# Optimization experiments

Measured on AMD Instinct MI355X. Metric: run time of the kernel, lower is better.

The kernel has to match this reference:

```python
import jax, jax.numpy as jnp
import numpy as np
from jax import lax

EPS = 1e-5

def conv2d(x, w, b, pad):
    y = lax.conv_general_dilated(x, w, (1, 1), [(pad, pad), (pad, pad)],
                                 dimension_numbers=('NCHW', 'OIHW', 'NCHW'))
    return y + b[None, :, None, None]

def batchnorm(x, gamma, beta):
    # training-mode BN (nn.Module default): biased batch stats over N,H,W
    m = x.mean((0, 2, 3), keepdims=True)
    v = x.var((0, 2, 3), keepdims=True)
    return (x - m) * lax.rsqrt(v + EPS) * gamma[None, :, None, None] + beta[None, :, None, None]

def mish(x):
    return x * jnp.tanh(jax.nn.softplus(x))

def haar_dwt2(y):
    # pywt.dwt2(..., 'haar', mode='zero') for even H,W: 2x2 block transform.
    # cA='aa', cH='da' (detail along rows axis), cV='ad', cD='dd'; scale 1/2.
    a = y[..., 0::2, 0::2]
    b = y[..., 0::2, 1::2]
    c = y[..., 1::2, 0::2]
    d = y[..., 1::2, 1::2]
    cA = (a + b + c + d) * 0.5
    cH = (a + b - c - d) * 0.5
    cV = (a - b + c - d) * 0.5
    cD = (a - b - c + d) * 0.5
    return cA, cH, cV, cD

def setup_inputs() -> dict:
    key = jax.random.key(0)
    ks = jax.random.split(key, 8)
    C = 64
    x = jax.random.normal(ks[0], (8, C, 256, 256), dtype=jnp.float32)
    def kaiming(k, shape):
        fan_in = int(np.prod(shape[1:]))
        return jax.random.normal(k, shape, dtype=jnp.float32) / np.sqrt(fan_in)
    return {
        'x': x,
        'w1': kaiming(ks[1], (2 * C, C, 3, 3)), 'b1': jnp.zeros((2 * C,), jnp.float32),
        'g1': jnp.ones((2 * C,), jnp.float32), 'be1': jnp.zeros((2 * C,), jnp.float32),
        'w2': kaiming(ks[2], (C, 2 * C, 3, 3)), 'b2': jnp.zeros((C,), jnp.float32),
        'g2': jnp.ones((C,), jnp.float32), 'be2': jnp.zeros((C,), jnp.float32),
        'wh': kaiming(ks[3], (C, 3 * C, 1, 1)), 'bh': jnp.zeros((C,), jnp.float32),
        'gh': jnp.ones((C,), jnp.float32), 'beh': jnp.zeros((C,), jnp.float32),
    }

def reference(x, w1, b1, g1, be1, w2, b2, g2, be2, wh, bh, gh, beh):
    residual = x
    h = mish(batchnorm(conv2d(x, w1, b1, 1), g1, be1))
    h = mish(batchnorm(conv2d(h, w2, b2, 1), g2, be2))
    y = h + residual
    # original SS_Block detaches before the DWT
    y = lax.stop_gradient(y)
    cA, cH, cV, cD = haar_dwt2(y)
    x_low = cA
    x_high = jnp.concatenate([cH, cV, cD], axis=1)  # [B, 3C, H/2, W/2]
    x_high = mish(batchnorm(conv2d(x_high, wh, bh, 0), gh, beh))
    return (x_low, x_high)
```

## Files before the change

kernel.cpp:

```cpp
#include <hip/hip_runtime.h>
#include <hip/hip_bf16.h>

#define DEV static __device__ __forceinline__

typedef short v8s __attribute__((ext_vector_type(8)));
typedef float v4f __attribute__((ext_vector_type(4)));
typedef unsigned short v4u __attribute__((ext_vector_type(4)));

constexpr int N_ = 8;
constexpr float EPS_ = 1e-5f;
constexpr float INV_CNT = 1.f / 524288.f;
constexpr int CHB = 12800;

constexpr int PB1 = 0;
constexpr int PB2 = 262144;
constexpr int PBH = 327680;


__device__ __align__(16) unsigned short g_wT1[9*128*64];
__device__ __align__(16) unsigned short g_wT2[9*64*128];
__device__ __align__(16) unsigned short g_whT[64*192];
__device__ __align__(16) float g_stats[512];
__device__ __align__(16) float g_part[458752];
__device__ __align__(16) unsigned short g_zero[64];

DEV float bfbits2f(unsigned short u) { return __uint_as_float(((unsigned)u) << 16); }
DEV unsigned short f2bfbits(float f) {
    __hip_bfloat16 h = __float2bfloat16(f);
    unsigned short b;
    __builtin_memcpy(&b, &h, 2);
    return b;
}

DEV float mishf(float v) {
    float t = __expf(fminf(v, 30.f));
    float num = fmaf(t, t, 2.f * t);
    return v * num * __builtin_amdgcn_rcpf(num + 2.f);
}

DEV void gll16(const unsigned short* g, unsigned short* l) {
    __builtin_amdgcn_global_load_lds(
        (const __attribute__((address_space(1))) unsigned int*)g,
        (__attribute__((address_space(3))) unsigned int*)l,
        16, 0, 0);
}

__global__ __launch_bounds__(256) void prep(const float* __restrict__ w1,
                                            const float* __restrict__ w2,
                                            const float* __restrict__ wh)
{
    int idx = blockIdx.x * 256 + threadIdx.x;
    if (idx < 512) g_stats[idx] = 0.f;
    if (idx < 64) g_zero[idx] = 0;
    if (idx < 12288) g_whT[idx] = f2bfbits(wh[idx]);
    if (idx < 73728) {
        int tap = idx / 8192, rem = idx & 8191;
        {   int oc = rem >> 6, ic = rem & 63;
            g_wT1[idx] = f2bfbits(w1[(oc * 64 + ic) * 9 + tap]); }
        {   int oc = rem >> 7, ic = rem & 127;
            g_wT2[idx] = f2bfbits(w2[(oc * 128 + ic) * 9 + tap]); }
    }
}

__global__ __launch_bounds__(256) void transpose_x(const float* __restrict__ x,
                                                   unsigned short* __restrict__ xh)
{
    __shared__ float t[64][65];
    const int tid = threadIdx.x;
    const int bid = blockIdx.x;
    const int n = bid >> 10, pb = bid & 1023;
    const size_t pix0 = (size_t)pb * 64;
    const float* xb = x + ((size_t)n << 22) + pix0;
#pragma unroll
    for (int cb = 0; cb < 4; ++cb) {
        int c = (tid >> 4) + cb * 16;
        int p = (tid & 15) * 4;
        float4 v = *(const float4*)(xb + ((size_t)c << 16) + p);
        t[c][p] = v.x; t[c][p+1] = v.y; t[c][p+2] = v.z; t[c][p+3] = v.w;
    }
    __syncthreads();
    unsigned short* ob = xh + (((size_t)n << 16) + pix0) * 64;
#pragma unroll
    for (int pb2 = 0; pb2 < 2; ++pb2) {
        int p = (tid >> 3) + pb2 * 32;
        int c0 = (tid & 7) * 8;
        v8s r;
#pragma unroll
        for (int i = 0; i < 8; ++i) r[i] = (short)f2bfbits(t[c0 + i][p]);
        *(v8s*)(ob + (size_t)p * 64 + c0) = r;
    }
}

__global__ __launch_bounds__(512, 2) void conv1MFMA(const unsigned short* __restrict__ in,
                                                    unsigned short* __restrict__ outp,
                                                    const int nTiles)
{
    __shared__ __align__(16) unsigned short Xs[3 * CHB + 512];
    const int tid  = threadIdx.x;
    const int lane = tid & 63;
    const int wv   = tid >> 6;
    const int pg   = (int)blockIdx.x;
    const int NPG  = (int)gridDim.x;

    const int ocw = wv >> 1;
    const int wp  = (wv & 1) * 32;
    const int l15 = lane & 15, kg = lane >> 4;

    v8s av[9][2][2];
    {
        const unsigned short* wb =
            g_wT1 + ((size_t)(ocw * 32 + l15)) * 64 + kg * 8;
#pragma unroll
        for (int tap = 0; tap < 9; ++tap)
#pragma unroll
            for (int ics = 0; ics < 2; ++ics)
#pragma unroll
                for (int sub = 0; sub < 2; ++sub)
                    av[tap][ics][sub] =
                        *(const v8s*)(wb + ((size_t)tap * 128 + sub * 16) * 64 + ics * 32);
    }

    auto stage = [&](int s) {
        const int pt   = pg + NPG * s;
        const int n    = pt >> 10;
        const int hrow = (pt >> 2) & 255;
        const int w0   = (pt & 3) * 64;
        unsigned short* buf = Xs + (s % 3) * CHB;
#pragma unroll
        for (int it = 0; it < 4; ++it) {
            const int cb = it * 512 + wv * 64;
            unsigned short* dst = (cb >= 1600) ? (Xs + 3 * CHB)
                                               : (buf + (size_t)cb * 8);
            const int chunk = cb + lane;
            int r   = chunk / 528;
            int rem = chunk - r * 528;
            int lc  = rem >> 3, k = rem & 7;
            int gr  = hrow - 1 + r;
            int gc  = w0 - 1 + lc;
            const unsigned short* src;
            if ((chunk < 1584) & ((unsigned)gr < 256u) & ((unsigned)gc < 256u))
                src = in + ((((size_t)n << 16) + ((size_t)gr << 8) + gc) * 64)
                         + ((k ^ (lc & 7)) << 3);
            else
                src = g_zero;
            gll16(src, dst);
        }
    };

    stage(0);
    stage(1);
    asm volatile("s_waitcnt vmcnt(4)" ::: "memory");
    __builtin_amdgcn_s_barrier();
    __builtin_amdgcn_sched_barrier(0);

    for (int s = 0; s < nTiles; ++s) {
        if (s + 2 < nTiles) stage(s + 2);

        const unsigned short* cur = Xs + (s % 3) * CHB;
        const int pt   = pg + NPG * s;
        const int n    = pt >> 10;
        const int hrow = (pt >> 2) & 255;
        const int w0   = (pt & 3) * 64;
        const size_t pixbase = ((size_t)n << 16) + ((size_t)hrow << 8) + w0;

        v4f acc[2][2];
        {
            v4f z = {0.f, 0.f, 0.f, 0.f};
            acc[0][0] = z; acc[0][1] = z; acc[1][0] = z; acc[1][1] = z;
        }
#pragma unroll
        for (int tap = 0; tap < 9; ++tap) {
            const int dyy = tap / 3, dxx = tap % 3;
            const int lc0 = wp + l15 + dxx;
#pragma unroll
            for (int ics = 0; ics < 2; ++ics) {
                const int off0 = ((dyy * 66 + lc0) * 8 + ((ics * 4 + kg) ^ (lc0 & 7))) * 8;
                v8s b0 = *(const v8s*)(cur + off0);
                v8s b1 = *(const v8s*)(cur + off0 + 16 * 64);
                acc[0][0] = __builtin_amdgcn_mfma_f32_16x16x32_bf16(av[tap][ics][0], b0, acc[0][0], 0, 0, 0);
                acc[1][0] = __builtin_amdgcn_mfma_f32_16x16x32_bf16(av[tap][ics][1], b0, acc[1][0], 0, 0, 0);
                acc[0][1] = __builtin_amdgcn_mfma_f32_16x16x32_bf16(av[tap][ics][0], b1, acc[0][1], 0, 0, 0);
                acc[1][1] = __builtin_amdgcn_mfma_f32_16x16x32_bf16(av[tap][ics][1], b1, acc[1][1], 0, 0, 0);
            }
        }

        if (s + 2 < nTiles) asm volatile("s_waitcnt vmcnt(4)" ::: "memory");
        else                asm volatile("s_waitcnt vmcnt(0)" ::: "memory");

#pragma unroll
        for (int sub = 0; sub < 2; ++sub)
#pragma unroll
            for (int ps = 0; ps < 2; ++ps) {
                const int px  = wp + ps * 16 + l15;
                const int ocb = ocw * 32 + sub * 16 + kg * 4;
                size_t gaddr = (pixbase + px) * 128 + ocb;
                v4f a = acc[sub][ps];
                v4u pk;
#pragma unroll
                for (int r = 0; r < 4; ++r) pk[r] = f2bfbits(a[r]);
                *(v4u*)(outp + gaddr) = pk;
            }

        __builtin_amdgcn_s_barrier();
        __builtin_amdgcn_sched_barrier(0);
    }
}

__global__ __launch_bounds__(512, 2) void conv2MFMA(const unsigned short* __restrict__ in,
                                                    unsigned short* __restrict__ outp,
                                                    const int nTiles)
{
    __shared__ __align__(16) unsigned short Xs[3 * CHB + 512];
    const int tid  = threadIdx.x;
    const int lane = tid & 63;
    const int wv   = tid >> 6;
    const int pg   = (int)blockIdx.x;
    const int NPG  = (int)gridDim.x;

    const int ocq = wv >> 1;
    const int wp  = (wv & 1) * 32;
    const int l15 = lane & 15, kg = lane >> 4;

    v8s av[9][4];
    {
        const unsigned short* wb =
            g_wT2 + ((size_t)(ocq * 16 + l15)) * 128 + kg * 8;
#pragma unroll
        for (int tap = 0; tap < 9; ++tap)
#pragma unroll
            for (int ics = 0; ics < 4; ++ics)
                av[tap][ics] = *(const v8s*)(wb + (size_t)tap * 64 * 128 + ics * 32);
    }

    auto stageH = [&](int s) {
        const int tt    = s >> 1;
        const int icoff = (s & 1) * 64;
        const int pt   = pg + NPG * tt;
        const int n    = pt >> 10;
        const int hrow = (pt >> 2) & 255;
        const int w0   = (pt & 3) * 64;
#pragma unroll
        for (int it = 0; it < 4; ++it) {
            const int cb = it * 512 + wv * 64;
            unsigned short* buf = Xs + (s % 3) * CHB;
            unsigned short* dst = (cb >= 1600) ? (Xs + 3 * CHB)
                                               : (buf + (size_t)cb * 8);
            const int chunk = cb + lane;
            int r   = chunk / 528;
            int rem = chunk - r * 528;
            int lc  = rem >> 3, k = rem & 7;
            int gr  = hrow - 1 + r;
            int gc  = w0 - 1 + lc;
            const unsigned short* src;
            if ((chunk < 1584) & ((unsigned)gr < 256u) & ((unsigned)gc < 256u))
                src = in + ((((size_t)n << 16) + ((size_t)gr << 8) + gc) * 128)
                         + icoff + ((k ^ (lc & 7)) << 3);
            else
                src = g_zero;
            gll16(src, dst);
        }
    };

    const int NS = nTiles * 2;
    stageH(0);
    stageH(1);
    asm volatile("s_waitcnt vmcnt(4)" ::: "memory");
    __builtin_amdgcn_s_barrier();
    __builtin_amdgcn_sched_barrier(0);

    for (int t = 0; t < nTiles; ++t) {
        const int s0 = 2 * t;
        v4f acc[2];
        {
            v4f z = {0.f, 0.f, 0.f, 0.f};
            acc[0] = z; acc[1] = z;
        }

        if (s0 + 2 < NS) stageH(s0 + 2);
        {
            const unsigned short* cur = Xs + (s0 % 3) * CHB;
#pragma unroll
            for (int tap = 0; tap < 9; ++tap) {
                const int dyy = tap / 3, dxx = tap % 3;
                const int lc0 = wp + l15 + dxx;
#pragma unroll
                for (int i2 = 0; i2 < 2; ++i2) {
                    const int off0 = ((dyy * 66 + lc0) * 8 + ((i2 * 4 + kg) ^ (lc0 & 7))) * 8;
                    v8s b0 = *(const v8s*)(cur + off0);
                    v8s b1 = *(const v8s*)(cur + off0 + 16 * 64);
                    acc[0] = __builtin_amdgcn_mfma_f32_16x16x32_bf16(av[tap][i2], b0, acc[0], 0, 0, 0);
                    acc[1] = __builtin_amdgcn_mfma_f32_16x16x32_bf16(av[tap][i2], b1, acc[1], 0, 0, 0);
                }
            }
        }
        if (s0 + 2 < NS) asm volatile("s_waitcnt vmcnt(4)" ::: "memory");
        else             asm volatile("s_waitcnt vmcnt(0)" ::: "memory");
        __builtin_amdgcn_s_barrier();
        __builtin_amdgcn_sched_barrier(0);

        if (s0 + 3 < NS) stageH(s0 + 3);
        {
            const unsigned short* cur = Xs + ((s0 + 1) % 3) * CHB;
#pragma unroll
            for (int tap = 0; tap < 9; ++tap) {
                const int dyy = tap / 3, dxx = tap % 3;
                const int lc0 = wp + l15 + dxx;
#pragma unroll
                for (int i2 = 0; i2 < 2; ++i2) {
                    const int off0 = ((dyy * 66 + lc0) * 8 + ((i2 * 4 + kg) ^ (lc0 & 7))) * 8;
                    v8s b0 = *(const v8s*)(cur + off0);
                    v8s b1 = *(const v8s*)(cur + off0 + 16 * 64);
                    acc[0] = __builtin_amdgcn_mfma_f32_16x16x32_bf16(av[tap][2 + i2], b0, acc[0], 0, 0, 0);
                    acc[1] = __builtin_amdgcn_mfma_f32_16x16x32_bf16(av[tap][2 + i2], b1, acc[1], 0, 0, 0);
                }
            }
        }
        if (s0 + 3 < NS) asm volatile("s_waitcnt vmcnt(4)" ::: "memory");
        else             asm volatile("s_waitcnt vmcnt(0)" ::: "memory");

        {
            const int pt   = pg + NPG * t;
            const int n    = pt >> 10;
            const int hrow = (pt >> 2) & 255;
            const int w0   = (pt & 3) * 64;
            const size_t gb = (size_t)(hrow & 1) * 16777216 + (size_t)n * 2097152
                            + (size_t)(hrow >> 1) * 256;
#pragma unroll
            for (int ps = 0; ps < 2; ++ps) {
                const int px = wp + ps * 16 + l15;
                const int wc = w0 + px;
                const int ocb = ocq * 16 + kg * 4;
                size_t gaddr = gb + (size_t)(wc >> 2) * 32768
                             + (size_t)((wc & 3) * 64 + ocb);
                v4u pk;
#pragma unroll
                for (int r = 0; r < 4; ++r) pk[r] = f2bfbits(acc[ps][r]);
                *(v4u*)(outp + gaddr) = pk;
            }
        }

        __builtin_amdgcn_s_barrier();
        __builtin_amdgcn_sched_barrier(0);
    }
}

template<int C, int PBASE>
__global__ __launch_bounds__(256) void statsP(const unsigned short* __restrict__ in, int P)
{
    constexpr int G = C / 8;
    constexpr int LG = (G == 16) ? 4 : 3;
    __shared__ float red[256 * 8];
    const int tid = threadIdx.x;
    const int cg = tid & (G - 1);
    float s[8], q[8];
#pragma unroll
    for (int j = 0; j < 8; ++j) { s[j] = 0.f; q[j] = 0.f; }
    const int tot = P * G;
    const int stride = gridDim.x * 256;
    for (int i = blockIdx.x * 256 + tid; i < tot; i += stride) {
        const int p = i >> LG;
        v8s v = *(const v8s*)(in + (size_t)p * C + cg * 8);
#pragma unroll
        for (int j = 0; j < 8; ++j) {
            float f = bfbits2f((unsigned short)v[j]);
            s[j] += f; q[j] = fmaf(f, f, q[j]);
        }
    }
#pragma unroll
    for (int j = 0; j < 8; ++j) red[tid * 8 + j] = s[j];
    __syncthreads();
    for (int st = (256 / G) >> 1; st > 0; st >>= 1) {
        if ((tid >> LG) < st)
#pragma unroll
            for (int j = 0; j < 8; ++j) red[tid * 8 + j] += red[(tid + st * G) * 8 + j];
        __syncthreads();
    }
    if (tid < G)
#pragma unroll
        for (int j = 0; j < 8; ++j)
            g_part[PBASE + blockIdx.x * (2 * C) + 2 * (cg * 8 + j)] = red[tid * 8 + j];
    __syncthreads();
#pragma unroll
    for (int j = 0; j < 8; ++j) red[tid * 8 + j] = q[j];
    __syncthreads();
    for (int st = (256 / G) >> 1; st > 0; st >>= 1) {
        if ((tid >> LG) < st)
#pragma unroll
            for (int j = 0; j < 8; ++j) red[tid * 8 + j] += red[(tid + st * G) * 8 + j];
        __syncthreads();
    }
    if (tid < G)
#pragma unroll
        for (int j = 0; j < 8; ++j)
            g_part[PBASE + blockIdx.x * (2 * C) + 2 * (cg * 8 + j) + 1] = red[tid * 8 + j];
}

template<int NV, int PBASE, int OFF>
__global__ __launch_bounds__(256) void statsR(int nparts)
{
    const int v = (int)blockIdx.x;
    float s = 0.f;
    for (int b = (int)threadIdx.x; b < nparts; b += 256)
        s += g_part[PBASE + b * NV + v];
    s += __shfl_down(s, 32); s += __shfl_down(s, 16);
    s += __shfl_down(s, 8);  s += __shfl_down(s, 4);
    s += __shfl_down(s, 2);  s += __shfl_down(s, 1);
    __shared__ float ls[4];
    if ((threadIdx.x & 63) == 0) ls[threadIdx.x >> 6] = s;
    __syncthreads();
    if (threadIdx.x == 0)
        g_stats[OFF + v] = ls[0] + ls[1] + ls[2] + ls[3];
}

template<int C, int OFF>
__global__ __launch_bounds__(256) void bnN(const unsigned short* __restrict__ in,
                                           unsigned short* __restrict__ outp,
                                           const float* __restrict__ gam,
                                           const float* __restrict__ bet, int total8)
{
    const int t0 = blockIdx.x * 256 + threadIdx.x;
    const int c0 = (t0 * 8) & (C - 1);
    float sc[8], sh[8];
#pragma unroll
    for (int j = 0; j < 8; ++j) {
        int c = c0 + j;
        float m  = g_stats[OFF + 2 * c] * INV_CNT;
        float va = fmaf(g_stats[OFF + 2 * c + 1], INV_CNT, -m * m);
        sc[j] = rsqrtf(va + EPS_) * gam[c];
        sh[j] = fmaf(-m, sc[j], bet[c]);
    }
    const int stride = gridDim.x * 256;
    for (int i = t0; i < total8; i += stride) {
        v8s v = *(const v8s*)(in + (size_t)i * 8);
        v8s o;
#pragma unroll
        for (int j = 0; j < 8; ++j)
            o[j] = (short)f2bfbits(mishf(fmaf(bfbits2f((unsigned short)v[j]), sc[j], sh[j])));
        *(v8s*)(outp + (size_t)i * 8) = o;
    }
}

__global__ __launch_bounds__(512) void haarFused(const unsigned short* c2,
                                                 const unsigned short* __restrict__ xh,
                                                 const float* __restrict__ g2,
                                                 const float* __restrict__ be2,
                                                 float* out_low,
                                                 float* convh)
{
    __shared__ __align__(16) unsigned short Bs[128 * 192];
    const int tid = threadIdx.x, lane = tid & 63;
    const int n = blockIdx.x >> 7, row = blockIdx.x & 127;

    const int wv = tid >> 6;
    const int ocw = wv >> 2, wp = (wv & 3) * 32;
    const int l15 = lane & 15, kg = lane >> 4;

    const int px = tid >> 2, cg = tid & 3;
    float low[16];
    v8s Hb[2], Vb[2], Db[2];
    {
        float sc[16], sh[16];
#pragma unroll
        for (int j = 0; j < 16; ++j) {
            int c = cg * 16 + j;
            float m  = g_stats[256 + 2 * c] * INV_CNT;
            float va = fmaf(g_stats[256 + 2 * c + 1], INV_CNT, -m * m);
            sc[j] = rsqrtf(va + EPS_) * g2[c];
            sh[j] = fmaf(-m, sc[j], be2[c]);
        }
        const size_t cbase = (size_t)n * 2097152 + (size_t)(px >> 1) * 32768
                           + (size_t)row * 256 + (px & 1) * 128 + cg * 16;
        const size_t xbase = ((size_t)n * 65536 + (size_t)(2 * row) * 256 + 2 * px) * 64 + cg * 16;
        v8s cv[2][2][2], xv[2][2][2];
#pragma unroll
        for (int i = 0; i < 2; ++i)
#pragma unroll
            for (int m = 0; m < 2; ++m) {
                const unsigned short* cp = c2 + cbase + (size_t)i * 16777216 + m * 64;
                cv[i][m][0] = *(const v8s*)cp;
                cv[i][m][1] = *(const v8s*)(cp + 8);
                const unsigned short* xp = xh + xbase + i * 16384 + m * 64;
                xv[i][m][0] = *(const v8s*)xp;
                xv[i][m][1] = *(const v8s*)(xp + 8);
            }
#pragma unroll
        for (int jj = 0; jj < 2; ++jj)
#pragma unroll
            for (int j = 0; j < 8; ++j) {
                const int jc = jj * 8 + j;
                float y00 = mishf(fmaf(bfbits2f((unsigned short)cv[0][0][jj][j]), sc[jc], sh[jc]))
                          + bfbits2f((unsigned short)xv[0][0][jj][j]);
                float y01 = mishf(fmaf(bfbits2f((unsigned short)cv[0][1][jj][j]), sc[jc], sh[jc]))
                          + bfbits2f((unsigned short)xv[0][1][jj][j]);
                float y10 = mishf(fmaf(bfbits2f((unsigned short)cv[1][0][jj][j]), sc[jc], sh[jc]))
                          + bfbits2f((unsigned short)xv[1][0][jj][j]);
                float y11 = mishf(fmaf(bfbits2f((unsigned short)cv[1][1][jj][j]), sc[jc], sh[jc]))
                          + bfbits2f((unsigned short)xv[1][1][jj][j]);
                low[jc] = 0.5f * (y00 + y01 + y10 + y11);
                Hb[jj][j] = (short)f2bfbits(0.5f * (y00 + y01 - y10 - y11));
                Vb[jj][j] = (short)f2bfbits(0.5f * (y00 - y01 + y10 - y11));
                Db[jj][j] = (short)f2bfbits(0.5f * (y00 - y01 - y10 + y11));
            }
        unsigned short* bp = Bs + px * 192;
        const int sx = px & 7;
#pragma unroll
        for (int jj = 0; jj < 2; ++jj) {
            *(v8s*)(bp + (((cg * 2 + jj) ^ sx) << 3))      = Hb[jj];
            *(v8s*)(bp + (((8 + cg * 2 + jj) ^ sx) << 3))  = Vb[jj];
            *(v8s*)(bp + (((16 + cg * 2 + jj) ^ sx) << 3)) = Db[jj];
        }
    }
    __syncthreads();

#pragma unroll
    for (int j = 0; j < 16; ++j) {
        const int c = cg * 16 + j;
        out_low[((size_t)(n * 64 + c) << 14) + row * 128 + px] = low[j];
    }

    v8s av2[6][2];
    {
        const unsigned short* wb = g_whT + (size_t)(ocw * 32 + l15) * 192 + kg * 8;
#pragma unroll
        for (int s = 0; s < 6; ++s)
#pragma unroll
            for (int sub = 0; sub < 2; ++sub)
                av2[s][sub] = *(const v8s*)(wb + (size_t)sub * 16 * 192 + s * 32);
    }

    v4f acc[2][2];
    {
        v4f z = {0.f, 0.f, 0.f, 0.f};
        acc[0][0] = z; acc[0][1] = z; acc[1][0] = z; acc[1][1] = z;
    }
    {
        const int pix0 = wp + l15;
        const unsigned short* bbase = Bs + pix0 * 192;
        const int sx0 = pix0 & 7;
#pragma unroll
        for (int s = 0; s < 6; ++s) {
            const int ck = s * 4 + kg;
            v8s b0 = *(const v8s*)(bbase + ((ck ^ sx0) << 3));
            v8s b1 = *(const v8s*)(bbase + 16 * 192 + ((ck ^ sx0) << 3));
            acc[0][0] = __builtin_amdgcn_mfma_f32_16x16x32_bf16(av2[s][0], b0, acc[0][0], 0, 0, 0);
            acc[1][0] = __builtin_amdgcn_mfma_f32_16x16x32_bf16(av2[s][1], b0, acc[1][0], 0, 0, 0);
            acc[0][1] = __builtin_amdgcn_mfma_f32_16x16x32_bf16(av2[s][0], b1, acc[0][1], 0, 0, 0);
            acc[1][1] = __builtin_amdgcn_mfma_f32_16x16x32_bf16(av2[s][1], b1, acc[1][1], 0, 0, 0);
        }
    }

    __syncthreads();
    float* Cf = (float*)Bs;
#pragma unroll
    for (int sub = 0; sub < 2; ++sub)
#pragma unroll
        for (int ps = 0; ps < 2; ++ps) {
            const int pxe = wp + ps * 16 + l15;
            const int ocb = ocw * 32 + sub * 16 + kg * 4;
#pragma unroll
            for (int r = 0; r < 4; ++r)
                Cf[(ocb + r) * 130 + pxe] = acc[sub][ps][r];
        }
    __syncthreads();
    {
        const int oc = tid >> 3, seg = tid & 7;
        float vals[16];
        float S = 0.f, Q = 0.f;
#pragma unroll
        for (int i = 0; i < 16; ++i) {
            float f = Cf[oc * 130 + seg * 16 + i];
            vals[i] = f; S += f; Q = fmaf(f, f, Q);
        }
        float* gp = convh + ((size_t)(n * 64 + oc) << 14) + row * 128 + seg * 16;
#pragma unroll
        for (int i4 = 0; i4 < 4; ++i4) {
            float4 t4;
            t4.x = vals[i4*4]; t4.y = vals[i4*4+1]; t4.z = vals[i4*4+2]; t4.w = vals[i4*4+3];
            *(float4*)(gp + i4 * 4) = t4;
        }
        S += __shfl_down(S, 4); Q += __shfl_down(Q, 4);
        S += __shfl_down(S, 2); Q += __shfl_down(Q, 2);
        S += __shfl_down(S, 1); Q += __shfl_down(Q, 1);
        if (seg == 0) {
            g_part[PBH + (size_t)blockIdx.x * 128 + 2 * oc]     = S;
            g_part[PBH + (size_t)blockIdx.x * 128 + 2 * oc + 1] = Q;
        }
    }
}

__global__ __launch_bounds__(256) void bnF(const float* __restrict__ in,
                                           float* __restrict__ outp, int stOff,
                                           const float* __restrict__ gam,
                                           const float* __restrict__ bet,
                                           int Cmask, int logHW, float invCnt, int total4)
{
    int t = blockIdx.x * 256 + threadIdx.x;
    if (t >= total4) return;
    int idx = t << 2;
    int c = (idx >> logHW) & Cmask;
    float mean = g_stats[stOff + 2 * c] * invCnt;
    float var = fmaf(g_stats[stOff + 2 * c + 1], invCnt, -mean * mean);
    float scale = rsqrtf(var + EPS_) * gam[c];
    float shift = fmaf(-mean, scale, bet[c]);
    float4 v = *(const float4*)(in + idx);
    v.x = mishf(fmaf(v.x, scale, shift));
    v.y = mishf(fmaf(v.y, scale, shift));
    v.z = mishf(fmaf(v.z, scale, shift));
    v.w = mishf(fmaf(v.w, scale, shift));
    *(float4*)(outp + idx) = v;
}

extern "C" void kernel_launch(void* const* d_in, const int* in_sizes, int n_in,
                              void* d_out, int out_size, void* d_ws, size_t ws_size,
                              hipStream_t stream)
{
    (void)in_sizes; (void)n_in; (void)out_size; (void)ws_size;

    const float* x   = (const float*)d_in[0];
    const float* w1  = (const float*)d_in[1];
    const float* g1  = (const float*)d_in[3];
    const float* be1 = (const float*)d_in[4];
    const float* w2  = (const float*)d_in[5];
    const float* g2  = (const float*)d_in[7];
    const float* be2 = (const float*)d_in[8];
    const float* wh  = (const float*)d_in[9];
    const float* gh  = (const float*)d_in[11];
    const float* beh = (const float*)d_in[12];

    char* ws = (char*)d_ws;
    unsigned short* xh = (unsigned short*)ws;
    unsigned short* h1 = (unsigned short*)(ws + 67108864);
    unsigned short* c2 = (unsigned short*)d_out;
    float* out_low = (float*)d_out;
    float* convh   = (float*)d_out + 8388608;

    prep<<<288, 256, 0, stream>>>(w1, w2, wh);
    transpose_x<<<8192, 256, 0, stream>>>(x, xh);

    conv1MFMA<<<1024, 512, 0, stream>>>(xh, h1, 8);
    statsP<128, PB1><<<1024, 256, 0, stream>>>(h1, 524288);
    statsR<256, PB1, 0><<<256, 256, 0, stream>>>(1024);
    bnN<128, 0><<<1024, 256, 0, stream>>>(h1, h1, g1, be1, 8388608);
    conv2MFMA<<<2048, 512, 0, stream>>>(h1, c2, 4);
    statsP<64, PB2><<<512, 256, 0, stream>>>(c2, 524288);
    statsR<128, PB2, 256><<<128, 256, 0, stream>>>(512);
    haarFused<<<1024, 512, 0, stream>>>(c2, xh, g2, be2, out_low, convh);
    statsR<128, PBH, 384><<<128, 256, 0, stream>>>(1024);
    bnF<<<8192, 256, 0, stream>>>(convh, convh, 384, gh, beh, 63, 14, 1.f / 131072.f, 2097152);
}
```

Measured before the change: 443.8 us.

## Retile conv2 MFMA kernel to two output rows per tile with 32-channel waves

conv2 now processes two output rows per tile, so the 4-row halo staged in LDS serves two rows instead of one and global/LDS input traffic per output drops. Each wave computes 32 output channels across two row/column sub-blocks, reusing each B fragment across two A fragments. Weight registers are halved by reloading each 64-channel half of the weights every tile. The triple-buffered vmcnt pipeline becomes a simpler double buffer with __syncthreads, and the grid is halved. The trade-off is repeated weight reloads from global/L2 and less overlap between staging and compute.

```diff
diff --git a/kernel.cpp b/kernel.cpp
--- a/kernel.cpp
+++ b/kernel.cpp
@@ -11,6 +11,7 @@
 constexpr float EPS_ = 1e-5f;
 constexpr float INV_CNT = 1.f / 524288.f;
 constexpr int CHB = 12800;
+constexpr int C2B = 16896;
 
 constexpr int PB1 = 0;
 constexpr int PB2 = 262144;
@@ -210,49 +211,50 @@
                                                     unsigned short* __restrict__ outp,
                                                     const int nTiles)
 {
-    __shared__ __align__(16) unsigned short Xs[3 * CHB + 512];
+    __shared__ __align__(16) unsigned short Xs[2 * C2B + 512];
     const int tid  = threadIdx.x;
     const int lane = tid & 63;
     const int wv   = tid >> 6;
     const int pg   = (int)blockIdx.x;
     const int NPG  = (int)gridDim.x;
 
-    const int ocq = wv >> 1;
+    const int ocw = wv >> 2;
+    const int ry  = (wv >> 1) & 1;
     const int wp  = (wv & 1) * 32;
     const int l15 = lane & 15, kg = lane >> 4;
 
-    v8s av[9][4];
-    {
+    v8s av[9][2][2];
+    auto loadW = [&](int icoff) {
         const unsigned short* wb =
-            g_wT2 + ((size_t)(ocq * 16 + l15)) * 128 + kg * 8;
+            g_wT2 + ((size_t)(ocw * 32 + l15)) * 128 + icoff + kg * 8;
 #pragma unroll
         for (int tap = 0; tap < 9; ++tap)
 #pragma unroll
-            for (int ics = 0; ics < 4; ++ics)
-                av[tap][ics] = *(const v8s*)(wb + (size_t)tap * 64 * 128 + ics * 32);
-    }
-
-    auto stageH = [&](int s) {
-        const int tt    = s >> 1;
-        const int icoff = (s & 1) * 64;
-        const int pt   = pg + NPG * tt;
-        const int n    = pt >> 10;
-        const int hrow = (pt >> 2) & 255;
-        const int w0   = (pt & 3) * 64;
-#pragma unroll
-        for (int it = 0; it < 4; ++it) {
+            for (int ics = 0; ics < 2; ++ics)
+#pragma unroll
+                for (int sub = 0; sub < 2; ++sub)
+                    av[tap][ics][sub] =
+                        *(const v8s*)(wb + ((size_t)tap * 64 + sub * 16) * 128 + ics * 32);
+    };
+
+    auto stageH = [&](int tt, int icoff, unsigned short* buf) {
+        const int pt    = pg + NPG * tt;
+        const int n     = pt >> 9;
+        const int hrow0 = ((pt >> 2) & 127) * 2;
+        const int w0    = (pt & 3) * 64;
+#pragma unroll
+        for (int it = 0; it < 5; ++it) {
             const int cb = it * 512 + wv * 64;
-            unsigned short* buf = Xs + (s % 3) * CHB;
-            unsigned short* dst = (cb >= 1600) ? (Xs + 3 * CHB)
+            unsigned short* dst = (cb >= 2112) ? (Xs + 2 * C2B)
                                                : (buf + (size_t)cb * 8);
             const int chunk = cb + lane;
             int r   = chunk / 528;
             int rem = chunk - r * 528;
             int lc  = rem >> 3, k = rem & 7;
-            int gr  = hrow - 1 + r;
+            int gr  = hrow0 - 1 + r;
             int gc  = w0 - 1 + lc;
             const unsigned short* src;
-            if ((chunk < 1584) & ((unsigned)gr < 256u) & ((unsigned)gc < 256u))
+            if ((chunk < 2112) & ((unsigned)gr < 256u) & ((unsigned)gc < 256u))
                 src = in + ((((size_t)n << 16) + ((size_t)gr << 8) + gc) * 128)
                          + icoff + ((k ^ (lc & 7)) << 3);
             else
@@ -261,86 +263,79 @@
         }
     };
 
-    const int NS = nTiles * 2;
-    stageH(0);
-    stageH(1);
-    asm volatile("s_waitcnt vmcnt(4)" ::: "memory");
-    __builtin_amdgcn_s_barrier();
-    __builtin_amdgcn_sched_barrier(0);
+    loadW(0);
+    stageH(0, 0, Xs);
+    __syncthreads();
 
     for (int t = 0; t < nTiles; ++t) {
-        const int s0 = 2 * t;
-        v4f acc[2];
+        v4f acc[2][2];
         {
             v4f z = {0.f, 0.f, 0.f, 0.f};
-            acc[0] = z; acc[1] = z;
-        }
-
-        if (s0 + 2 < NS) stageH(s0 + 2);
+            acc[0][0] = z; acc[0][1] = z; acc[1][0] = z; acc[1][1] = z;
+        }
+
+        stageH(t, 64, Xs + C2B);
+#pragma unroll
+        for (int tap = 0; tap < 9; ++tap) {
+            const int dyy = tap / 3, dxx = tap % 3;
+            const int lrow = ry + dyy;
+            const int lc0 = wp + l15 + dxx;
+#pragma unroll
+            for (int ics = 0; ics < 2; ++ics) {
+                const int off0 = ((lrow * 66 + lc0) * 8 + ((ics * 4 + kg) ^ (lc0 & 7))) * 8;
+                v8s b0 = *(const v8s*)(Xs + off0);
+                v8s b1 = *(const v8s*)(Xs + off0 + 16 * 64);
+                acc[0][0] = __builtin_amdgcn_mfma_f32_16x16x32_bf16(av[tap][ics][0], b0, acc[0][0], 0, 0, 0);
+                acc[1][0] = __builtin_amdgcn_mfma_f32_16x16x32_bf16(av[tap][ics][1], b0, acc[1][0], 0, 0, 0);
+                acc[0][1] = __builtin_amdgcn_mfma_f32_16x16x32_bf16(av[tap][ics][0], b1, acc[0][1], 0, 0, 0);
+                acc[1][1] = __builtin_amdgcn_mfma_f32_16x16x32_bf16(av[tap][ics][1], b1, acc[1][1], 0, 0, 0);
+            }
+        }
+        __syncthreads();
+
+        if (t + 1 < nTiles) stageH(t + 1, 0, Xs);
+        loadW(64);
+#pragma unroll
+        for (int tap = 0; tap < 9; ++tap) {
+            const int dyy = tap / 3, dxx = tap % 3;
+            const int lrow = ry + dyy;
+            const int lc0 = wp + l15 + dxx;
+#pragma unroll
+            for (int ics = 0; ics < 2; ++ics) {
+                const int off0 = ((lrow * 66 + lc0) * 8 + ((ics * 4 + kg) ^ (lc0 & 7))) * 8;
+                v8s b0 = *(const v8s*)(Xs + C2B + off0);
+                v8s b1 = *(const v8s*)(Xs + C2B + off0 + 16 * 64);
+                acc[0][0] = __builtin_amdgcn_mfma_f32_16x16x32_bf16(av[tap][ics][0], b0, acc[0][0], 0, 0, 0);
+                acc[1][0] = __builtin_amdgcn_mfma_f32_16x16x32_bf16(av[tap][ics][1], b0, acc[1][0], 0, 0, 0);
+                acc[0][1] = __builtin_amdgcn_mfma_f32_16x16x32_bf16(av[tap][ics][0], b1, acc[0][1], 0, 0, 0);
+                acc[1][1] = __builtin_amdgcn_mfma_f32_16x16x32_bf16(av[tap][ics][1], b1, acc[1][1], 0, 0, 0);
+            }
+        }
+
         {
-            const unsigned short* cur = Xs + (s0 % 3) * CHB;
-#pragma unroll
-            for (int tap = 0; tap < 9; ++tap) {
-                const int dyy = tap / 3, dxx = tap % 3;
-                const int lc0 = wp + l15 + dxx;
-#pragma unroll
-                for (int i2 = 0; i2 < 2; ++i2) {
-                    const int off0 = ((dyy * 66 + lc0) * 8 + ((i2 * 4 + kg) ^ (lc0 & 7))) * 8;
-                    v8s b0 = *(const v8s*)(cur + off0);
-                    v8s b1 = *(const v8s*)(cur + off0 + 16 * 64);
-                    acc[0] = __builtin_amdgcn_mfma_f32_16x16x32_bf16(av[tap][i2], b0, acc[0], 0, 0, 0);
-                    acc[1] = __builtin_amdgcn_mfma_f32_16x16x32_bf16(av[tap][i2], b1, acc[1], 0, 0, 0);
+            const int pt    = pg + NPG * t;
+            const int n     = pt >> 9;
+            const int rowpr = (pt >> 2) & 127;
+            const int w0    = (pt & 3) * 64;
+            const size_t gb = (size_t)ry * 16777216 + (size_t)n * 2097152
+                            + (size_t)rowpr * 256;
+#pragma unroll
+            for (int sub = 0; sub < 2; ++sub)
+#pragma unroll
+                for (int ps = 0; ps < 2; ++ps) {
+                    const int wc  = w0 + wp + ps * 16 + l15;
+                    const int ocb = ocw * 32 + sub * 16 + kg * 4;
+                    size_t gaddr = gb + (size_t)(wc >> 2) * 32768
+                                 + (size_t)((wc & 3) * 64 + ocb);
+                    v4u pk;
+#pragma unroll
+                    for (int r = 0; r < 4; ++r) pk[r] = f2bfbits(acc[sub][ps][r]);
+                    *(v4u*)(outp + gaddr) = pk;
                 }
-            }
-        }
-        if (s0 + 2 < NS) asm volatile("s_waitcnt vmcnt(4)" ::: "memory");
-        else             asm volatile("s_waitcnt vmcnt(0)" ::: "memory");
-        __builtin_amdgcn_s_barrier();
-        __builtin_amdgcn_sched_barrier(0);
-
-        if (s0 + 3 < NS) stageH(s0 + 3);
-        {
-            const unsigned short* cur = Xs + ((s0 + 1) % 3) * CHB;
-#pragma unroll
-            for (int tap = 0; tap < 9; ++tap) {
-                const int dyy = tap / 3, dxx = tap % 3;
-                const int lc0 = wp + l15 + dxx;
-#pragma unroll
-                for (int i2 = 0; i2 < 2; ++i2) {
-                    const int off0 = ((dyy * 66 + lc0) * 8 + ((i2 * 4 + kg) ^ (lc0 & 7))) * 8;
-                    v8s b0 = *(const v8s*)(cur + off0);
-                    v8s b1 = *(const v8s*)(cur + off0 + 16 * 64);
-                    acc[0] = __builtin_amdgcn_mfma_f32_16x16x32_bf16(av[tap][2 + i2], b0, acc[0], 0, 0, 0);
-                    acc[1] = __builtin_amdgcn_mfma_f32_16x16x32_bf16(av[tap][2 + i2], b1, acc[1], 0, 0, 0);
-                }
-            }
-        }
-        if (s0 + 3 < NS) asm volatile("s_waitcnt vmcnt(4)" ::: "memory");
-        else             asm volatile("s_waitcnt vmcnt(0)" ::: "memory");
-
-        {
-            const int pt   = pg + NPG * t;
-            const int n    = pt >> 10;
-            const int hrow = (pt >> 2) & 255;
-            const int w0   = (pt & 3) * 64;
-            const size_t gb = (size_t)(hrow & 1) * 16777216 + (size_t)n * 2097152
-                            + (size_t)(hrow >> 1) * 256;
-#pragma unroll
-            for (int ps = 0; ps < 2; ++ps) {
-                const int px = wp + ps * 16 + l15;
-                const int wc = w0 + px;
-                const int ocb = ocq * 16 + kg * 4;
-                size_t gaddr = gb + (size_t)(wc >> 2) * 32768
-                             + (size_t)((wc & 3) * 64 + ocb);
-                v4u pk;
-#pragma unroll
-                for (int r = 0; r < 4; ++r) pk[r] = f2bfbits(acc[ps][r]);
-                *(v4u*)(outp + gaddr) = pk;
-            }
-        }
-
-        __builtin_amdgcn_s_barrier();
-        __builtin_amdgcn_sched_barrier(0);
+        }
+
+        loadW(0);
+        __syncthreads();
     }
 }
 
@@ -641,7 +636,7 @@
     statsP<128, PB1><<<1024, 256, 0, stream>>>(h1, 524288);
     statsR<256, PB1, 0><<<256, 256, 0, stream>>>(1024);
     bnN<128, 0><<<1024, 256, 0, stream>>>(h1, h1, g1, be1, 8388608);
-    conv2MFMA<<<2048, 512, 0, stream>>>(h1, c2, 4);
+    conv2MFMA<<<1024, 512, 0, stream>>>(h1, c2, 4);
     statsP<64, PB2><<<512, 256, 0, stream>>>(c2, 524288);
     statsR<128, PB2, 256><<<128, 256, 0, stream>>>(512);
     haarFused<<<1024, 512, 0, stream>>>(c2, xh, g2, be2, out_low, convh);
```

Measured after the change: 783.1 us. 76.5% more time.
